# Kernel optimization log

Measured on AMD Instinct MI355X. Metric: run time of the kernel, lower is better.

Reference implementation:

```python
import jax, jax.numpy as jnp
import numpy as np

N_NODES = 10000
N_EDGES = 80000
TILE, EMB, HID, OUT = 32, 128, 256, 512


def setup_inputs() -> dict:
    key = jax.random.key(0)
    ks = jax.random.split(key, 20)
    s = 0.05
    inp = {
        'x': jax.random.normal(ks[0], (N_NODES, TILE), dtype=jnp.float32),
        'edge_index': jax.random.randint(ks[1], (2, N_EDGES), 0, N_NODES, dtype=jnp.int64),
        # input_proj (spectral_norm Linear -> treated as a plain normalized weight)
        'W_in': jax.random.normal(ks[2], (TILE, EMB), dtype=jnp.float32) * s,
        'b_in': jnp.zeros((EMB,), dtype=jnp.float32),
        # GATConv 1: 128 -> 256, heads=8
        'W1': jax.random.normal(ks[3], (EMB, 8 * HID), dtype=jnp.float32) * s,
        'as1': jax.random.normal(ks[4], (8, HID), dtype=jnp.float32) * s,
        'ad1': jax.random.normal(ks[5], (8, HID), dtype=jnp.float32) * s,
        'b1': jnp.zeros((8 * HID,), dtype=jnp.float32),
        # GATConv 2: 2048 -> 256, heads=8
        'W2': jax.random.normal(ks[6], (8 * HID, 8 * HID), dtype=jnp.float32) * s,
        'as2': jax.random.normal(ks[7], (8, HID), dtype=jnp.float32) * s,
        'ad2': jax.random.normal(ks[8], (8, HID), dtype=jnp.float32) * s,
        'b2': jnp.zeros((8 * HID,), dtype=jnp.float32),
        # GATConv 3: 2048 -> 512, heads=1
        'W3': jax.random.normal(ks[9], (8 * HID, OUT), dtype=jnp.float32) * s,
        'as3': jax.random.normal(ks[10], (1, OUT), dtype=jnp.float32) * s,
        'ad3': jax.random.normal(ks[11], (1, OUT), dtype=jnp.float32) * s,
        'b3': jnp.zeros((OUT,), dtype=jnp.float32),
    }
    return inp


def _gat(x, src, dst, W, a_src, a_dst, bias, heads, ch):
    # x: [N, F_in]; src/dst: [E_tot] (self loops included)
    n = x.shape[0]
    h = (x @ W).reshape(n, heads, ch)                      # [N, H, C]
    alpha_src = jnp.sum(h * a_src, axis=-1)                # [N, H]
    alpha_dst = jnp.sum(h * a_dst, axis=-1)                # [N, H]
    e = jax.nn.leaky_relu(alpha_src[src] + alpha_dst[dst], 0.2)  # [E, H]
    # segment softmax over destination nodes
    m = jax.ops.segment_max(e, dst, num_segments=n)
    ex = jnp.exp(e - m[dst])
    denom = jax.ops.segment_sum(ex, dst, num_segments=n)
    alpha = ex / (denom[dst] + 1e-16)                      # [E, H]
    out = jax.ops.segment_sum(h[src] * alpha[:, :, None], dst, num_segments=n)
    return out.reshape(n, heads * ch) + bias


def reference(x, edge_index, W_in, b_in, W1, as1, ad1, b1, W2, as2, ad2, b2, W3, as3, ad3, b3):
    n = x.shape[0]
    lr = lambda t: jax.nn.leaky_relu(t, 0.2)
    # PyG GATConv adds self-loops by default
    loops = jnp.arange(n, dtype=edge_index.dtype)
    src = jnp.concatenate([edge_index[0], loops])
    dst = jnp.concatenate([edge_index[1], loops])
    h = lr(x @ W_in + b_in)
    h = lr(_gat(h, src, dst, W1, as1, ad1, b1, 8, HID))
    h = lr(_gat(h, src, dst, W2, as2, ad2, b2, 8, HID))
    h = lr(_gat(h, src, dst, W3, as3, ad3, b3, 1, OUT))
    return h
```

## Files before the change

### kernel.cpp

```cpp
#include <hip/hip_runtime.h>

typedef unsigned short u16;
typedef unsigned int u32;
typedef _Float16 f16;
typedef f16 f16x8 __attribute__((ext_vector_type(8)));
typedef float f32x4 __attribute__((ext_vector_type(4)));

__device__ __forceinline__ float h2f(f16 h){ return (float)h; }
__device__ __forceinline__ f16 f2h(float f){ return (f16)f; }

__device__ __forceinline__ f16x8 ldfrag(const f16* p){
  union { uint4 u; f16x8 h; } x;
  x.u = *(const uint4*)p;
  return x.h;
}
__device__ __forceinline__ void gload_lds16(const f16* g, f16* l){
  __builtin_amdgcn_global_load_lds(
      (const __attribute__((address_space(1))) u32*)g,
      (__attribute__((address_space(3))) u32*)l, 16, 0, 0);
}

template<int N> __device__ __forceinline__ void wait_vmcnt(){
  if constexpr      (N == 0) asm volatile("s_waitcnt vmcnt(0)" ::: "memory");
  else if constexpr (N == 2) asm volatile("s_waitcnt vmcnt(2)" ::: "memory");
  else if constexpr (N == 4) asm volatile("s_waitcnt vmcnt(4)" ::: "memory");
  else if constexpr (N == 6) asm volatile("s_waitcnt vmcnt(6)" ::: "memory");
  else if constexpr (N == 8) asm volatile("s_waitcnt vmcnt(8)" ::: "memory");
  else static_assert(N == 0, "unsupported vmcnt");
}


__global__ void detect_kernel(const int* __restrict__ ei, int* __restrict__ flag){
  if (threadIdx.x == 0 && blockIdx.x == 0){
    int orv = 0;
    for (int i = 0; i < 200; i++) orv |= ei[2*i + 1];
    *flag = (orv == 0) ? 1 : 0;
  }
}

__global__ void init_kernel(int* __restrict__ cnt, int* __restrict__ fillpos, int n){
  int i = blockIdx.x * blockDim.x + threadIdx.x;
  if (i < n){ cnt[i] = 1; fillpos[i] = 1; }
}

__global__ void count_edges(const int* __restrict__ ei, int E, const int* __restrict__ flag,
                            int* __restrict__ cnt){
  int e = blockIdx.x * blockDim.x + threadIdx.x;
  if (e >= E) return;
  int dst = (*flag) ? ei[2*E + 2*e] : ei[E + e];
  atomicAdd(&cnt[dst], 1);
}

#define SCAN_T 1024
__global__ void scan_kernel(const int* __restrict__ cnt, int* __restrict__ row_ptr, int n){
  __shared__ int sm[SCAN_T];
  int t = threadIdx.x;
  int chunk = (n + SCAN_T - 1) / SCAN_T;
  int lo = t * chunk, hi = lo + chunk; if (hi > n) hi = n; if (lo > n) lo = n;
  int s = 0;
  for (int i = lo; i < hi; i++) s += cnt[i];
  sm[t] = s; __syncthreads();
  for (int off = 1; off < SCAN_T; off <<= 1){
    int v = (t >= off) ? sm[t - off] : 0;
    __syncthreads();
    sm[t] += v;
    __syncthreads();
  }
  int base = sm[t] - s;
  for (int i = lo; i < hi; i++){ row_ptr[i] = base; base += cnt[i]; }
  if (t == 0) row_ptr[n] = sm[SCAN_T - 1];
}

__global__ void selfloop_kernel(const int* __restrict__ row_ptr, int* __restrict__ col, int n){
  int i = blockIdx.x * blockDim.x + threadIdx.x;
  if (i < n) col[row_ptr[i]] = i;
}

__global__ void fill_edges(const int* __restrict__ ei, int E, const int* __restrict__ flag,
                           const int* __restrict__ row_ptr, int* __restrict__ fillpos,
                           int* __restrict__ col){
  int e = blockIdx.x * blockDim.x + threadIdx.x;
  if (e >= E) return;
  int f = *flag;
  int src = f ? ei[2*e]       : ei[e];
  int dst = f ? ei[2*E + 2*e] : ei[E + e];
  int off = atomicAdd(&fillpos[dst], 1);
  col[row_ptr[dst] + off] = src;
}


__global__ void convert_f16(const float* __restrict__ X, f16* __restrict__ Xo, long n){
  long i = blockIdx.x * (long)blockDim.x + threadIdx.x;
  if (i >= n) return;
  Xo[i] = f2h(X[i]);
}

__global__ void convert_wT(const float* __restrict__ W, f16* __restrict__ T, int K, int N){
  __shared__ float sm[32][33];
  int kb = blockIdx.x * 32, nb = blockIdx.y * 32;
  int tx = threadIdx.x, ty = threadIdx.y;
  for (int i = 0; i < 32; i += 8)
    sm[ty + i][tx] = W[(size_t)(kb + ty + i) * N + nb + tx];
  __syncthreads();
  for (int i = 0; i < 32; i += 8)
    T[(size_t)(nb + ty + i) * K + kb + tx] = f2h(sm[tx][ty + i]);
}


template<int EPI, int FJ, int BK>
__global__ __launch_bounds__(256) void gemm_kernel(
    const f16* __restrict__ A, const f16* __restrict__ B,
    float* __restrict__ C, f16* __restrict__ Ch,
    const float* __restrict__ bias,
    int M, int N, int K, int nbm, int nbn)
{
  constexpr int BN  = FJ * 32;
  constexpr int TPR = BK / 8;
  constexpr int RPG = 256 / TPR;
  constexpr int NGA = 128 / RPG;
  constexpr int NGB = BN / RPG;
  constexpr int KS  = BK / 32;
  constexpr int NL  = NGA + NGB;

  __shared__ f16 sA[2][128 * BK];
  __shared__ f16 sB[2][BN * BK];

  int nwg = nbm * nbn;
  int bid = blockIdx.x;
  int q = nwg >> 3, r = nwg & 7;
  int xcd = bid & 7, idx = bid >> 3;
  int wg = (xcd < r ? xcd * (q + 1) : r * (q + 1) + (xcd - r) * q) + idx;
  int bm = wg / nbn, bn = wg % nbn;

  int tid = threadIdx.x;
  int lane = tid & 63;
  int w = tid >> 6;
  int wr = (w >> 1) * 64, wc = (w & 1) * (FJ * 16);
  int lm = lane & 15;

  int slot = tid % TPR, rg = tid / TPR;
  int sk;
  if constexpr (BK == 64) sk = ((slot ^ (rg & 7))) * 8;
  else                    sk = ((slot ^ ((rg >> 1) & 3))) * 8;

  const f16* pA[NGA];
  const f16* pB[NGB];
  #pragma unroll
  for (int i = 0; i < NGA; i++)
    pA[i] = A + ((long)bm * 128 + rg + RPG * i) * K + sk;
  #pragma unroll
  for (int i = 0; i < NGB; i++)
    pB[i] = B + ((long)bn * BN + rg + RPG * i) * K + sk;

  auto STAGE = [&](int buf, int k0){
    #pragma unroll
    for (int i = 0; i < NGA; i++)
      gload_lds16(pA[i] + k0, &sA[buf][i * 2048 + tid * 8]);
    #pragma unroll
    for (int i = 0; i < NGB; i++)
      gload_lds16(pB[i] + k0, &sB[buf][i * 2048 + tid * 8]);
  };

  f32x4 acc[4][FJ] = {};

  int nt = K / BK;
  STAGE(0, 0);
  int cur = 0;
  for (int t = 0; t < nt; t++){
    if (t + 1 < nt){
      STAGE(cur ^ 1, (t + 1) * BK);
      wait_vmcnt<NL>();
    } else {
      wait_vmcnt<0>();
    }
    __builtin_amdgcn_s_barrier();
    __builtin_amdgcn_sched_barrier(0);

    f16x8 af[4][KS], bfr[FJ][KS];
    #pragma unroll
    for (int ks = 0; ks < KS; ks++){
      #pragma unroll
      for (int f = 0; f < 4; f++){
        int row = wr + f * 16 + lm;
        int phys;
        if constexpr (BK == 64) phys = (ks * 4 + (lane >> 4)) ^ (lm & 7);
        else                    phys = (lane >> 4) ^ ((lm >> 1) & 3);
        af[f][ks] = ldfrag(&sA[cur][row * BK + phys * 8]);
      }
      #pragma unroll
      for (int f = 0; f < FJ; f++){
        int row = wc + f * 16 + lm;
        int phys;
        if constexpr (BK == 64) phys = (ks * 4 + (lane >> 4)) ^ (lm & 7);
        else                    phys = (lane >> 4) ^ ((lm >> 1) & 3);
        bfr[f][ks] = ldfrag(&sB[cur][row * BK + phys * 8]);
      }
    }
    __builtin_amdgcn_s_setprio(1);
    #pragma unroll
    for (int ks = 0; ks < KS; ks++)
      #pragma unroll
      for (int fi = 0; fi < 4; fi++)
        #pragma unroll
        for (int fj = 0; fj < FJ; fj++)
          acc[fi][fj] = __builtin_amdgcn_mfma_f32_16x16x32_f16(
              af[fi][ks], bfr[fj][ks], acc[fi][fj], 0, 0, 0);
    __builtin_amdgcn_s_setprio(0);
    __builtin_amdgcn_sched_barrier(0);
    __builtin_amdgcn_s_barrier();
    cur ^= 1;
  }

  #pragma unroll
  for (int fi = 0; fi < 4; fi++){
    int mb = bm * 128 + wr + fi * 16 + ((lane >> 4) << 2);
    #pragma unroll
    for (int fj = 0; fj < FJ; fj++){
      int n = bn * BN + wc + fj * 16 + lm;
      #pragma unroll
      for (int j = 0; j < 4; j++){
        int m = mb + j;
        float v = acc[fi][fj][j];
        size_t o = (size_t)m * N + n;
        if (EPI == 0){
          C[o] = v;
        } else if (EPI == 2){
          Ch[o] = f2h(v);
        } else {
          v += bias[n];
          v = v > 0.0f ? v : 0.2f * v;
          Ch[o] = f2h(v);
        }
      }
    }
  }
}


template<int HEADS, int CH>
__global__ __launch_bounds__(256) void alpha_kernel(
    const f16* __restrict__ H, const float* __restrict__ a_s, const float* __restrict__ a_d,
    float* __restrict__ asrc, float* __restrict__ adst, int Nn)
{
  int gw = blockIdx.x * 4 + (threadIdx.x >> 6);
  int lane = threadIdx.x & 63;
  int node = gw / HEADS, hd = gw % HEADS;
  if (node >= Nn) return;
  size_t base = (size_t)node * HEADS * CH + hd * CH;
  const float* asp = a_s + hd * CH;
  const float* adp = a_d + hd * CH;
  float s1 = 0.0f, s2 = 0.0f;
  #pragma unroll
  for (int i = 0; i < CH / 256; i++){
    int off = i * 256 + lane * 4;
    union { uint2 u; f16 h[4]; } x;
    x.u = *(const uint2*)(H + base + off);
    float4 s4 = *(const float4*)(asp + off);
    float4 d4 = *(const float4*)(adp + off);
    s1 += h2f(x.h[0]) * s4.x + h2f(x.h[1]) * s4.y + h2f(x.h[2]) * s4.z + h2f(x.h[3]) * s4.w;
    s2 += h2f(x.h[0]) * d4.x + h2f(x.h[1]) * d4.y + h2f(x.h[2]) * d4.z + h2f(x.h[3]) * d4.w;
  }
  for (int off = 32; off; off >>= 1){
    s1 += __shfl_xor(s1, off);
    s2 += __shfl_xor(s2, off);
  }
  if (lane == 0){ asrc[gw] = s1; adst[gw] = s2; }
}


template<int HEADS, int CH, bool FINAL>
__global__ __launch_bounds__(256) void smax_agg_kernel(
    const f16* __restrict__ H, const int* __restrict__ row_ptr,
    const int* __restrict__ col,
    const float* __restrict__ asrc, const float* __restrict__ adst,
    const float* __restrict__ bias, f16* __restrict__ Oh, float* __restrict__ Ofp)
{
  constexpr int F = HEADS * CH;
  constexpr int CPT = F / 256;
  __shared__ float s_m[HEADS], s_inv[HEADS];
  int dst = blockIdx.x;
  int t = threadIdx.x;
  int s = row_ptr[dst], e = row_ptr[dst + 1];

  if (t < 64){
    const int hd = (HEADS == 8) ? (t & 7) : 0;
    const int el = (HEADS == 8) ? (t >> 3) : t;
    const int EPP = 64 / HEADS;
    float ad = adst[dst * HEADS + hd];
    float m = -1e30f;
    for (int p = s + el; p < e; p += EPP){
      float v = asrc[col[p] * HEADS + hd] + ad;
      v = v > 0.0f ? v : 0.2f * v;
      m = fmaxf(m, v);
    }
    for (int off = HEADS; off < 64; off <<= 1) m = fmaxf(m, __shfl_xor(m, off));
    float sum = 0.0f;
    for (int p = s + el; p < e; p += EPP){
      float v = asrc[col[p] * HEADS + hd] + ad;
      v = v > 0.0f ? v : 0.2f * v;
      sum += __expf(v - m);
    }
    for (int off = HEADS; off < 64; off <<= 1) sum += __shfl_xor(sum, off);
    if (el == 0){ s_m[hd] = m; s_inv[hd] = 1.0f / (sum + 1e-16f); }
  }
  __syncthreads();

  int c0 = t * CPT;
  int hd = c0 / CH;
  float m = s_m[hd], inv = s_inv[hd];
  float ad = adst[dst * HEADS + hd];
  float acc[CPT] = {};
  int p = s;

  auto wgt = [&](int src) -> float {
    float v = asrc[src * HEADS + hd] + ad;
    v = v > 0.0f ? v : 0.2f * v;
    return __expf(v - m) * inv;
  };

  for (; p + 4 <= e; p += 4){
    int i0 = col[p], i1 = col[p+1], i2 = col[p+2], i3 = col[p+3];
    if (CPT == 8){
      union { uint4 u; f16 h[8]; } x0, x1, x2, x3;
      x0.u = *(const uint4*)(H + (size_t)i0 * F + c0);
      x1.u = *(const uint4*)(H + (size_t)i1 * F + c0);
      x2.u = *(const uint4*)(H + (size_t)i2 * F + c0);
      x3.u = *(const uint4*)(H + (size_t)i3 * F + c0);
      float w0 = wgt(i0), w1 = wgt(i1), w2 = wgt(i2), w3 = wgt(i3);
      #pragma unroll
      for (int i = 0; i < 8; i++)
        acc[i] += w0 * h2f(x0.h[i]) + w1 * h2f(x1.h[i])
                + w2 * h2f(x2.h[i]) + w3 * h2f(x3.h[i]);
    } else {
      union { u32 u; f16 h[2]; } x0, x1, x2, x3;
      x0.u = *(const u32*)(H + (size_t)i0 * F + c0);
      x1.u = *(const u32*)(H + (size_t)i1 * F + c0);
      x2.u = *(const u32*)(H + (size_t)i2 * F + c0);
      x3.u = *(const u32*)(H + (size_t)i3 * F + c0);
      float w0 = wgt(i0), w1 = wgt(i1), w2 = wgt(i2), w3 = wgt(i3);
      acc[0] += w0 * h2f(x0.h[0]) + w1 * h2f(x1.h[0]) + w2 * h2f(x2.h[0]) + w3 * h2f(x3.h[0]);
      acc[1] += w0 * h2f(x0.h[1]) + w1 * h2f(x1.h[1]) + w2 * h2f(x2.h[1]) + w3 * h2f(x3.h[1]);
    }
  }
  for (; p < e; p++){
    int src = col[p];
    float w0 = wgt(src);
    if (CPT == 8){
      union { uint4 u; f16 h[8]; } x;
      x.u = *(const uint4*)(H + (size_t)src * F + c0);
      #pragma unroll
      for (int i = 0; i < 8; i++) acc[i] += w0 * h2f(x.h[i]);
    } else {
      union { u32 u; f16 h[2]; } x;
      x.u = *(const u32*)(H + (size_t)src * F + c0);
      acc[0] += w0 * h2f(x.h[0]); acc[1] += w0 * h2f(x.h[1]);
    }
  }

  #pragma unroll
  for (int i = 0; i < CPT; i++){
    float v = acc[i] + bias[c0 + i];
    v = v > 0.0f ? v : 0.2f * v;
    size_t o = (size_t)dst * F + c0 + i;
    if (FINAL) Ofp[o] = v;
    else       Oh[o]  = f2h(v);
  }
}


extern "C" void kernel_launch(void* const* d_in, const int* in_sizes, int n_in,
                              void* d_out, int out_size, void* d_ws, size_t ws_size,
                              hipStream_t stream)
{
  const float* x    = (const float*)d_in[0];
  const int*   ei   = (const int*)d_in[1];
  const float* W_in = (const float*)d_in[2];
  const float* b_in = (const float*)d_in[3];
  const float* W1   = (const float*)d_in[4];
  const float* as1  = (const float*)d_in[5];
  const float* ad1  = (const float*)d_in[6];
  const float* b1   = (const float*)d_in[7];
  const float* W2   = (const float*)d_in[8];
  const float* as2  = (const float*)d_in[9];
  const float* ad2  = (const float*)d_in[10];
  const float* b2   = (const float*)d_in[11];
  const float* W3   = (const float*)d_in[12];
  const float* as3  = (const float*)d_in[13];
  const float* ad3  = (const float*)d_in[14];
  const float* b3   = (const float*)d_in[15];

  const int N  = in_sizes[0] / 32;
  const int E  = in_sizes[1] / 2;
  const int ET = E + N;
  const int MT = (N + 127) / 128;
  const int MP = MT * 128;

  char* w = (char*)d_ws;
  size_t off = 0;
  auto carve = [&](size_t bytes) -> char* {
    off = (off + 255) & ~(size_t)255;
    char* p = w + off;
    off += bytes;
    return p;
  };

  int* flag    = (int*)carve(4);
  int* cnt     = (int*)carve((size_t)N * 4);
  int* fillpos = (int*)carve((size_t)N * 4);
  int* row_ptr = (int*)carve((size_t)(N + 1) * 4);
  int* col     = (int*)carve((size_t)ET * 4);
  f16* xh      = (f16*)carve((size_t)MP * 32 * 2);
  f16* h0      = (f16*)carve((size_t)MP * 128 * 2);
  f16* WT      = (f16*)carve((size_t)2048 * 2048 * 2);
  f16* Hb      = (f16*)carve((size_t)MP * 2048 * 2);
  f16* H3      = (f16*)carve((size_t)MP * 512 * 2);
  f16* XB      = (f16*)carve((size_t)MP * 2048 * 2);
  float* asrc  = (float*)carve((size_t)N * 8 * 4);
  float* adst  = (float*)carve((size_t)N * 8 * 4);

  if (off > ws_size) return;

  float* out = (float*)d_out;

  detect_kernel<<<1, 1, 0, stream>>>(ei, flag);
  init_kernel<<<(N + 255) / 256, 256, 0, stream>>>(cnt, fillpos, N);
  count_edges<<<(E + 255) / 256, 256, 0, stream>>>(ei, E, flag, cnt);
  scan_kernel<<<1, SCAN_T, 0, stream>>>(cnt, row_ptr, N);
  selfloop_kernel<<<(N + 255) / 256, 256, 0, stream>>>(row_ptr, col, N);
  fill_edges<<<(E + 255) / 256, 256, 0, stream>>>(ei, E, flag, row_ptr, fillpos, col);

  convert_f16<<<((long)N * 32 + 255) / 256, 256, 0, stream>>>(x, xh, (long)N * 32);
  convert_wT<<<dim3(1, 4), dim3(32, 8), 0, stream>>>(W_in, WT, 32, 128);
  gemm_kernel<1, 4, 32><<<MT * 1, 256, 0, stream>>>(xh, WT, nullptr, h0, b_in,
      MP, 128, 32, MT, 1);

  convert_wT<<<dim3(4, 64), dim3(32, 8), 0, stream>>>(W1, WT, 128, 2048);
  gemm_kernel<2, 4, 32><<<MT * 16, 256, 0, stream>>>(h0, WT, nullptr, Hb, nullptr,
      MP, 2048, 128, MT, 16);
  alpha_kernel<8, 256><<<(N * 8 + 3) / 4, 256, 0, stream>>>(Hb, as1, ad1, asrc, adst, N);
  smax_agg_kernel<8, 256, false><<<N, 256, 0, stream>>>(Hb, row_ptr, col,
      asrc, adst, b1, XB, nullptr);

  convert_wT<<<dim3(64, 64), dim3(32, 8), 0, stream>>>(W2, WT, 2048, 2048);
  gemm_kernel<2, 4, 32><<<MT * 16, 256, 0, stream>>>(XB, WT, nullptr, Hb, nullptr,
      MP, 2048, 2048, MT, 16);
  alpha_kernel<8, 256><<<(N * 8 + 3) / 4, 256, 0, stream>>>(Hb, as2, ad2, asrc, adst, N);
  smax_agg_kernel<8, 256, false><<<N, 256, 0, stream>>>(Hb, row_ptr, col,
      asrc, adst, b2, XB, nullptr);

  convert_wT<<<dim3(64, 16), dim3(32, 8), 0, stream>>>(W3, WT, 2048, 512);
  gemm_kernel<2, 2, 64><<<MT * 8, 256, 0, stream>>>(XB, WT, nullptr, H3, nullptr,
      MP, 512, 2048, MT, 8);
  alpha_kernel<1, 512><<<(N + 3) / 4, 256, 0, stream>>>(H3, as3, ad3, asrc, adst, N);
  smax_agg_kernel<1, 512, true><<<N, 256, 0, stream>>>(H3, row_ptr, col,
      asrc, adst, b3, nullptr, out);
}
```

Baseline: 366.7 us.

## Fuse attention-score dot products into GEMM epilogue and batch prep kernels

Computes the per-head attention dot products (h·a_src, h·a_dst) from the GEMM accumulators in the epilogue and writes per-tile partial sums, which a small reduce kernel then combines. This removes the separate alpha pass that re-read the full f16 feature matrix after each layer. It also merges the input conversion and all four weight transposes into one launch with separate weight buffers, and merges several CSR-building kernels, to cut launch count. In exchange the scores are taken from fp32 accumulators instead of the rounded f16 outputs, and the GEMM epilogue gets extra shuffles and register pressure.

Result: slower. 377.6 us (+3.0%).

```diff
diff --git a/kernel.cpp b/kernel.cpp
--- a/kernel.cpp
+++ b/kernel.cpp
@@ -30,16 +30,14 @@
 }
 
 
-__global__ void detect_kernel(const int* __restrict__ ei, int* __restrict__ flag){
-  if (threadIdx.x == 0 && blockIdx.x == 0){
+__global__ void csr_init(const int* __restrict__ ei, int* __restrict__ flag,
+                         int* __restrict__ cnt, int* __restrict__ fillpos, int n){
+  int i = blockIdx.x * blockDim.x + threadIdx.x;
+  if (i == 0){
     int orv = 0;
-    for (int i = 0; i < 200; i++) orv |= ei[2*i + 1];
+    for (int k = 0; k < 200; k++) orv |= ei[2*k + 1];
     *flag = (orv == 0) ? 1 : 0;
   }
-}
-
-__global__ void init_kernel(int* __restrict__ cnt, int* __restrict__ fillpos, int n){
-  int i = blockIdx.x * blockDim.x + threadIdx.x;
   if (i < n){ cnt[i] = 1; fillpos[i] = 1; }
 }
 
@@ -71,34 +69,45 @@
   if (t == 0) row_ptr[n] = sm[SCAN_T - 1];
 }
 
-__global__ void selfloop_kernel(const int* __restrict__ row_ptr, int* __restrict__ col, int n){
+__global__ void loop_fill(const int* __restrict__ ei, int E, const int* __restrict__ flag,
+                          const int* __restrict__ row_ptr, int* __restrict__ fillpos,
+                          int* __restrict__ col, int n){
   int i = blockIdx.x * blockDim.x + threadIdx.x;
   if (i < n) col[row_ptr[i]] = i;
-}
-
-__global__ void fill_edges(const int* __restrict__ ei, int E, const int* __restrict__ flag,
-                           const int* __restrict__ row_ptr, int* __restrict__ fillpos,
-                           int* __restrict__ col){
-  int e = blockIdx.x * blockDim.x + threadIdx.x;
-  if (e >= E) return;
-  int f = *flag;
-  int src = f ? ei[2*e]       : ei[e];
-  int dst = f ? ei[2*E + 2*e] : ei[E + e];
-  int off = atomicAdd(&fillpos[dst], 1);
-  col[row_ptr[dst] + off] = src;
-}
-
-
-__global__ void convert_f16(const float* __restrict__ X, f16* __restrict__ Xo, long n){
-  long i = blockIdx.x * (long)blockDim.x + threadIdx.x;
-  if (i >= n) return;
-  Xo[i] = f2h(X[i]);
-}
-
-__global__ void convert_wT(const float* __restrict__ W, f16* __restrict__ T, int K, int N){
+  if (i < E){
+    int f = *flag;
+    int src = f ? ei[2*i]       : ei[i];
+    int dst = f ? ei[2*E + 2*i] : ei[E + i];
+    int off = atomicAdd(&fillpos[dst], 1);
+    col[row_ptr[dst] + off] = src;
+  }
+}
+
+
+__global__ __launch_bounds__(256) void prep_kernel(
+    const float* __restrict__ x, f16* __restrict__ xh, int nx, int nbx,
+    const float* __restrict__ Win, f16* __restrict__ Twin,
+    const float* __restrict__ W1, f16* __restrict__ T1,
+    const float* __restrict__ W2, f16* __restrict__ T2,
+    const float* __restrict__ W3, f16* __restrict__ T3)
+{
+  int b = blockIdx.x;
+  int tid = threadIdx.x;
+  if (b < nbx){
+    int i = b * 256 + tid;
+    if (i < nx) xh[i] = f2h(x[i]);
+    return;
+  }
+  b -= nbx;
+  const float* W; f16* T; int K, N;
+  if (b < 4)              { W = Win; T = Twin; K = 32;   N = 128;  }
+  else if ((b -= 4) < 256){ W = W1;  T = T1;   K = 128;  N = 2048; }
+  else if ((b -= 256) < 4096){ W = W2; T = T2; K = 2048; N = 2048; }
+  else { b -= 4096;         W = W3;  T = T3;   K = 2048; N = 512;  }
+  int kbn = K / 32;
+  int kb = (b % kbn) * 32, nb = (b / kbn) * 32;
   __shared__ float sm[32][33];
-  int kb = blockIdx.x * 32, nb = blockIdx.y * 32;
-  int tx = threadIdx.x, ty = threadIdx.y;
+  int tx = tid & 31, ty = tid >> 5;
   for (int i = 0; i < 32; i += 8)
     sm[ty + i][tx] = W[(size_t)(kb + ty + i) * N + nb + tx];
   __syncthreads();
@@ -107,11 +116,13 @@
 }
 
 
-template<int EPI, int FJ, int BK>
+template<int EPI, int FJ, int BK, bool FA>
 __global__ __launch_bounds__(256) void gemm_kernel(
     const f16* __restrict__ A, const f16* __restrict__ B,
     float* __restrict__ C, f16* __restrict__ Ch,
     const float* __restrict__ bias,
+    const float* __restrict__ asf, const float* __restrict__ adf,
+    float* __restrict__ part,
     int M, int N, int K, int nbm, int nbn)
 {
   constexpr int BN  = FJ * 32;
@@ -234,37 +245,64 @@
       }
     }
   }
-}
-
-
-template<int HEADS, int CH>
-__global__ __launch_bounds__(256) void alpha_kernel(
-    const f16* __restrict__ H, const float* __restrict__ a_s, const float* __restrict__ a_d,
-    float* __restrict__ asrc, float* __restrict__ adst, int Nn)
+
+  if constexpr (FA){
+    int wcIdx = w & 1;
+    float av[FJ], dv[FJ];
+    #pragma unroll
+    for (int fj = 0; fj < FJ; fj++){
+      int n = bn * BN + wc + fj * 16 + lm;
+      av[fj] = asf[n];
+      dv[fj] = adf[n];
+    }
+    #pragma unroll
+    for (int fi = 0; fi < 4; fi++){
+      #pragma unroll
+      for (int j = 0; j < 4; j++){
+        float pa = 0.0f, pd = 0.0f;
+        #pragma unroll
+        for (int fj = 0; fj < FJ; fj++){
+          float v = acc[fi][fj][j];
+          pa += v * av[fj];
+          pd += v * dv[fj];
+        }
+        #pragma unroll
+        for (int mk = 1; mk < 16; mk <<= 1){
+          pa += __shfl_xor(pa, mk);
+          pd += __shfl_xor(pd, mk);
+        }
+        if (lm == 0){
+          int m = bm * 128 + wr + fi * 16 + ((lane >> 4) << 2) + j;
+          float* pp = part + ((size_t)m * 64 + bn * 4 + wcIdx * 2);
+          pp[0] = pa;
+          pp[1] = pd;
+        }
+      }
+    }
+  }
+}
+
+
+template<int HEADS>
+__global__ __launch_bounds__(256) void alpha_reduce(
+    const float* __restrict__ part, float* __restrict__ asrc,
+    float* __restrict__ adst, int Nn, int nbn)
 {
-  int gw = blockIdx.x * 4 + (threadIdx.x >> 6);
-  int lane = threadIdx.x & 63;
-  int node = gw / HEADS, hd = gw % HEADS;
-  if (node >= Nn) return;
-  size_t base = (size_t)node * HEADS * CH + hd * CH;
-  const float* asp = a_s + hd * CH;
-  const float* adp = a_d + hd * CH;
-  float s1 = 0.0f, s2 = 0.0f;
-  #pragma unroll
-  for (int i = 0; i < CH / 256; i++){
-    int off = i * 256 + lane * 4;
-    union { uint2 u; f16 h[4]; } x;
-    x.u = *(const uint2*)(H + base + off);
-    float4 s4 = *(const float4*)(asp + off);
-    float4 d4 = *(const float4*)(adp + off);
-    s1 += h2f(x.h[0]) * s4.x + h2f(x.h[1]) * s4.y + h2f(x.h[2]) * s4.z + h2f(x.h[3]) * s4.w;
-    s2 += h2f(x.h[0]) * d4.x + h2f(x.h[1]) * d4.y + h2f(x.h[2]) * d4.z + h2f(x.h[3]) * d4.w;
-  }
-  for (int off = 32; off; off >>= 1){
-    s1 += __shfl_xor(s1, off);
-    s2 += __shfl_xor(s2, off);
-  }
-  if (lane == 0){ asrc[gw] = s1; adst[gw] = s2; }
+  int idx = blockIdx.x * blockDim.x + threadIdx.x;
+  if (idx >= Nn * HEADS) return;
+  int node = idx / HEADS, hd = idx % HEADS;
+  int bn0 = (HEADS == 8) ? 2 * hd     : 0;
+  int bn1 = (HEADS == 8) ? 2 * hd + 2 : nbn;
+  float sa = 0.0f, sd = 0.0f;
+  for (int bn = bn0; bn < bn1; bn++)
+    #pragma unroll
+    for (int wci = 0; wci < 2; wci++){
+      const float* pp = part + ((size_t)node * 64 + bn * 4 + wci * 2);
+      sa += pp[0];
+      sd += pp[1];
+    }
+  asrc[idx] = sa;
+  adst[idx] = sd;
 }
 
 
@@ -411,47 +449,50 @@
   int* col     = (int*)carve((size_t)ET * 4);
   f16* xh      = (f16*)carve((size_t)MP * 32 * 2);
   f16* h0      = (f16*)carve((size_t)MP * 128 * 2);
-  f16* WT      = (f16*)carve((size_t)2048 * 2048 * 2);
+  f16* Twin    = (f16*)carve((size_t)128 * 32 * 2);
+  f16* T1      = (f16*)carve((size_t)2048 * 128 * 2);
+  f16* T2      = (f16*)carve((size_t)2048 * 2048 * 2);
+  f16* T3      = (f16*)carve((size_t)512 * 2048 * 2);
   f16* Hb      = (f16*)carve((size_t)MP * 2048 * 2);
   f16* H3      = (f16*)carve((size_t)MP * 512 * 2);
   f16* XB      = (f16*)carve((size_t)MP * 2048 * 2);
+  float* part  = (float*)carve((size_t)MP * 64 * 4);
   float* asrc  = (float*)carve((size_t)N * 8 * 4);
   float* adst  = (float*)carve((size_t)N * 8 * 4);
 
   if (off > ws_size) return;
 
   float* out = (float*)d_out;
-
-  detect_kernel<<<1, 1, 0, stream>>>(ei, flag);
-  init_kernel<<<(N + 255) / 256, 256, 0, stream>>>(cnt, fillpos, N);
+  const int nbx = (N * 32 + 255) / 256;
+  const int prep_grid = nbx + 4 + 256 + 4096 + 1024;
+  const int lf_grid = ((E > N ? E : N) + 255) / 256;
+
+  prep_kernel<<<prep_grid, 256, 0, stream>>>(x, xh, N * 32, nbx,
+      W_in, Twin, W1, T1, W2, T2, W3, T3);
+
+  csr_init<<<(N + 255) / 256, 256, 0, stream>>>(ei, flag, cnt, fillpos, N);
   count_edges<<<(E + 255) / 256, 256, 0, stream>>>(ei, E, flag, cnt);
   scan_kernel<<<1, SCAN_T, 0, stream>>>(cnt, row_ptr, N);
-  selfloop_kernel<<<(N + 255) / 256, 256, 0, stream>>>(row_ptr, col, N);
-  fill_edges<<<(E + 255) / 256, 256, 0, stream>>>(ei, E, flag, row_ptr, fillpos, col);
-
-  convert_f16<<<((long)N * 32 + 255) / 256, 256, 0, stream>>>(x, xh, (long)N * 32);
-  convert_wT<<<dim3(1, 4), dim3(32, 8), 0, stream>>>(W_in, WT, 32, 128);
-  gemm_kernel<1, 4, 32><<<MT * 1, 256, 0, stream>>>(xh, WT, nullptr, h0, b_in,
-      MP, 128, 32, MT, 1);
-
-  convert_wT<<<dim3(4, 64), dim3(32, 8), 0, stream>>>(W1, WT, 128, 2048);
-  gemm_kernel<2, 4, 32><<<MT * 16, 256, 0, stream>>>(h0, WT, nullptr, Hb, nullptr,
-      MP, 2048, 128, MT, 16);
-  alpha_kernel<8, 256><<<(N * 8 + 3) / 4, 256, 0, stream>>>(Hb, as1, ad1, asrc, adst, N);
+  loop_fill<<<lf_grid, 256, 0, stream>>>(ei, E, flag, row_ptr, fillpos, col, N);
+
+  gemm_kernel<1, 4, 32, false><<<MT * 1, 256, 0, stream>>>(xh, Twin, nullptr, h0,
+      b_in, nullptr, nullptr, nullptr, MP, 128, 32, MT, 1);
+
+  gemm_kernel<2, 4, 32, true><<<MT * 16, 256, 0, stream>>>(h0, T1, nullptr, Hb,
+      nullptr, as1, ad1, part, MP, 2048, 128, MT, 16);
+  alpha_reduce<8><<<(N * 8 + 255) / 256, 256, 0, stream>>>(part, asrc, adst, N, 16);
   smax_agg_kernel<8, 256, false><<<N, 256, 0, stream>>>(Hb, row_ptr, col,
       asrc, adst, b1, XB, nullptr);
 
-  convert_wT<<<dim3(64, 64), dim3(32, 8), 0, stream>>>(W2, WT, 2048, 2048);
-  gemm_kernel<2, 4, 32><<<MT * 16, 256, 0, stream>>>(XB, WT, nullptr, Hb, nullptr,
-      MP, 2048, 2048, MT, 16);
-  alpha_kernel<8, 256><<<(N * 8 + 3) / 4, 256, 0, stream>>>(Hb, as2, ad2, asrc, adst, N);
+  gemm_kernel<2, 4, 32, true><<<MT * 16, 256, 0, stream>>>(XB, T2, nullptr, Hb,
+      nullptr, as2, ad2, part, MP, 2048, 2048, MT, 16);
+  alpha_reduce<8><<<(N * 8 + 255) / 256, 256, 0, stream>>>(part, asrc, adst, N, 16);
   smax_agg_kernel<8, 256, false><<<N, 256, 0, stream>>>(Hb, row_ptr, col,
       asrc, adst, b2, XB, nullptr);
 
-  convert_wT<<<dim3(64, 16), dim3(32, 8), 0, stream>>>(W3, WT, 2048, 512);
-  gemm_kernel<2, 2, 64><<<MT * 8, 256, 0, stream>>>(XB, WT, nullptr, H3, nullptr,
-      MP, 512, 2048, MT, 8);
-  alpha_kernel<1, 512><<<(N + 3) / 4, 256, 0, stream>>>(H3, as3, ad3, asrc, adst, N);
+  gemm_kernel<2, 2, 64, true><<<MT * 8, 256, 0, stream>>>(XB, T3, nullptr, H3,
+      nullptr, as3, ad3, part, MP, 512, 2048, MT, 8);
+  alpha_reduce<1><<<(N + 255) / 256, 256, 0, stream>>>(part, asrc, adst, N, 8);
   smax_agg_kernel<1, 512, true><<<N, 256, 0, stream>>>(H3, row_ptr, col,
       asrc, adst, b3, nullptr, out);
 }
```
